# Kernel tuning notes

Hardware: AMD Instinct MI355X
Metric: run time of the kernel (lower is better)

Reference implementation:

```python
import jax, jax.numpy as jnp
import numpy as np

B, S, F, H, DK = 16, 1024, 512, 8, 64
NEG = 999999.0

def setup_inputs() -> dict:
    key = jax.random.key(0)
    ks = jax.random.split(key, 10)
    s = 1.0 / np.sqrt(F)
    inp = {
        'x': jax.random.normal(ks[0], (B, S, F), dtype=jnp.float32),
        'xlen': jax.random.randint(ks[1], (B,), 1, S + 1, dtype=jnp.int32),
        'WQw': jax.random.uniform(ks[2], (H, DK, F), jnp.float32, -s, s),
        'WQb': jax.random.uniform(ks[3], (H, DK), jnp.float32, -s, s),
        'WKw': jax.random.uniform(ks[4], (H, DK, F), jnp.float32, -s, s),
        'WKb': jax.random.uniform(ks[5], (H, DK), jnp.float32, -s, s),
        'WVw': jax.random.uniform(ks[6], (H, DK, F), jnp.float32, -s, s),
        'WVb': jax.random.uniform(ks[7], (H, DK), jnp.float32, -s, s),
        'WOw': jax.random.uniform(ks[8], (F, H * DK), jnp.float32, -1.0/np.sqrt(H*DK), 1.0/np.sqrt(H*DK)),
        'WOb': jax.random.uniform(ks[9], (F,), jnp.float32, -1.0/np.sqrt(H*DK), 1.0/np.sqrt(H*DK)),
    }
    return inp

def reference(x, xlen, WQw, WQb, WKw, WKb, WVw, WVb, WOw, WOb):
    # batched per-head projections: [B,S,F] x [H,DK,F] -> [B,H,S,DK]
    q = jnp.einsum('bsf,hdf->bhsd', x, WQw) + WQb[None, :, None, :]
    k = jnp.einsum('bsf,hdf->bhsd', x, WKw) + WKb[None, :, None, :]
    v = jnp.einsum('bsf,hdf->bhsd', x, WVw) + WVb[None, :, None, :]
    scores = jnp.einsum('bhsd,bhtd->bhst', q, k) / jnp.sqrt(jnp.float32(DK))
    # additive padding mask; original masks key positions >= xlen[j]-1 (off-by-one preserved)
    key_pos = jnp.arange(S)[None, :]                       # [1,S]
    mask = jnp.where(key_pos >= (xlen - 1)[:, None], -NEG, 0.0).astype(jnp.float32)
    scores = scores + mask[:, None, None, :]               # [B,H,S,S]
    attn = jax.nn.softmax(scores, axis=-1)
    z = jnp.einsum('bhst,bhtd->bhsd', attn, v)             # [B,H,S,DK]
    z = jnp.transpose(z, (0, 2, 1, 3)).reshape(B, S, H * DK)  # concat heads
    return z @ WOw.T + WOb
```

## Files before the change

kernel.cpp:

```cpp
#include <hip/hip_runtime.h>
#include <hip/hip_bf16.h>

typedef short bf16x8 __attribute__((ext_vector_type(8)));
typedef float f32x4 __attribute__((ext_vector_type(4)));
typedef unsigned short u16;

#define B_   16
#define S_   1024
#define F_   512
#define H_   8
#define DK_  64


__device__ __forceinline__ u16 f2bf(float f) {
    union { float f; unsigned int u; } v; v.f = f;
    return (u16)((v.u + 0x7FFFu + ((v.u >> 16) & 1u)) >> 16);
}
__device__ __forceinline__ float bf2f(u16 h) {
    union { unsigned int u; float f; } v; v.u = ((unsigned int)h) << 16;
    return v.f;
}
__device__ __forceinline__ bf16x8 cvt8(float4 a, float4 b) {
    union { u16 u[8]; bf16x8 v; } r;
    r.u[0] = f2bf(a.x); r.u[1] = f2bf(a.y); r.u[2] = f2bf(a.z); r.u[3] = f2bf(a.w);
    r.u[4] = f2bf(b.x); r.u[5] = f2bf(b.y); r.u[6] = f2bf(b.z); r.u[7] = f2bf(b.w);
    return r.v;
}
__device__ __forceinline__ unsigned int pk2(float lo, float hi) {
    union { __hip_bfloat162 h; unsigned int u; } c;
    c.h = __float22bfloat162_rn(make_float2(lo, hi));
    return c.u;
}

__device__ __forceinline__ void gl_lds16(const u16* g, u16* l) {
    __builtin_amdgcn_global_load_lds(
        (const __attribute__((address_space(1))) unsigned int*)g,
        (__attribute__((address_space(3))) unsigned int*)l,
        16, 0, 0);
}

__global__ __launch_bounds__(256) void cvt_all(
    const float* __restrict__ x,
    const float* __restrict__ wq, const float* __restrict__ wk,
    const float* __restrict__ wv, const float* __restrict__ wo,
    const float* __restrict__ bq, const float* __restrict__ bk,
    const float* __restrict__ bv, const float* __restrict__ bo,
    u16* __restrict__ Xbf, u16* __restrict__ Wbase)
{
    const size_t u = (size_t)blockIdx.x * 256 + threadIdx.x;
    const float* src; u16* dst;
    if (u < 1048576)      { src = x  + u * 8;               dst = Xbf + u * 8; }
    else if (u < 1081344) { src = wq + (u - 1048576) * 8;   dst = Wbase + (u - 1048576) * 8; }
    else if (u < 1114112) { src = wk + (u - 1081344) * 8;   dst = Wbase +  262144 + (u - 1081344) * 8; }
    else if (u < 1146880) { src = wv + (u - 1114112) * 8;   dst = Wbase +  524288 + (u - 1114112) * 8; }
    else if (u < 1179648) { src = wo + (u - 1146880) * 8;   dst = Wbase +  786432 + (u - 1146880) * 8; }
    else if (u < 1179712) { src = bq + (u - 1179648) * 8;   dst = Wbase + 1048576 + (u - 1179648) * 8; }
    else if (u < 1179776) { src = bk + (u - 1179712) * 8;   dst = Wbase + 1049088 + (u - 1179712) * 8; }
    else if (u < 1179840) { src = bv + (u - 1179776) * 8;   dst = Wbase + 1049600 + (u - 1179776) * 8; }
    else                  { src = bo + (u - 1179840) * 8;   dst = Wbase + 1050112 + (u - 1179840) * 8; }
    *(bf16x8*)dst = cvt8(*(const float4*)src, *(const float4*)(src + 4));
}

template <int EPI>
__global__ __launch_bounds__(256) void gemm128(
    const u16* __restrict__ A, const u16* __restrict__ Bm,
    const u16* __restrict__ bias, void* __restrict__ out)
{
    __shared__ __align__(16) u16 AsL[2][4096];
    __shared__ __align__(16) u16 BsL[2][4096];

    const int t    = threadIdx.x;
    const int wave = t >> 6, lane = t & 63;
    const int l15  = lane & 15, quad = lane >> 4;
    const int wr   = (wave & 1) * 64, wc = (wave >> 1) * 64;
    const int m0   = blockIdx.x * 128, n0 = blockIdx.y * 128;
    const int sr   = t >> 2, scol = (t & 3) * 8;

    float bvp[4];
#pragma unroll
    for (int j = 0; j < 4; j++) bvp[j] = bf2f(bias[n0 + wc + j * 16 + l15]);

    f32x4 acc[4][4];
#pragma unroll
    for (int i = 0; i < 4; i++)
#pragma unroll
        for (int j = 0; j < 4; j++) acc[i][j] = {0.f, 0.f, 0.f, 0.f};

    const u16* Ab = A  + (size_t)(m0 + sr) * 512 + scol;
    const u16* Bb = Bm + (size_t)(n0 + sr) * 512 + scol;

    gl_lds16(Ab,              &AsL[0][t * 8]);
    gl_lds16(Ab + 32768,      &AsL[0][2048 + t * 8]);
    gl_lds16(Bb,              &BsL[0][t * 8]);
    gl_lds16(Bb + 32768,      &BsL[0][2048 + t * 8]);
    gl_lds16(Ab + 32,         &AsL[1][t * 8]);
    gl_lds16(Ab + 32768 + 32, &AsL[1][2048 + t * 8]);
    gl_lds16(Bb + 32,         &BsL[1][t * 8]);
    gl_lds16(Bb + 32768 + 32, &BsL[1][2048 + t * 8]);

    for (int t0 = 0; t0 < 15; ++t0) {
        asm volatile("s_waitcnt vmcnt(4)" ::: "memory");
        __builtin_amdgcn_s_barrier();
        __builtin_amdgcn_sched_barrier(0);
        const int c = t0 & 1;
        bf16x8 af[4], bfv[4];
#pragma unroll
        for (int i = 0; i < 4; i++) af[i]  = *(const bf16x8*)&AsL[c][(wr + i * 16 + l15) * 32 + quad * 8];
#pragma unroll
        for (int j = 0; j < 4; j++) bfv[j] = *(const bf16x8*)&BsL[c][(wc + j * 16 + l15) * 32 + quad * 8];
#pragma unroll
        for (int i = 0; i < 4; i++)
#pragma unroll
            for (int j = 0; j < 4; j++)
                acc[i][j] = __builtin_amdgcn_mfma_f32_16x16x32_bf16(af[i], bfv[j], acc[i][j], 0, 0, 0);
        __builtin_amdgcn_sched_barrier(0);
        __builtin_amdgcn_s_barrier();
        if (t0 < 14) {
            const int k0n = (t0 + 2) * 32;
            gl_lds16(Ab + k0n,         &AsL[c][t * 8]);
            gl_lds16(Ab + 32768 + k0n, &AsL[c][2048 + t * 8]);
            gl_lds16(Bb + k0n,         &BsL[c][t * 8]);
            gl_lds16(Bb + 32768 + k0n, &BsL[c][2048 + t * 8]);
        }
    }
    asm volatile("s_waitcnt vmcnt(0)" ::: "memory");
    __builtin_amdgcn_s_barrier();
    __builtin_amdgcn_sched_barrier(0);
    {
        bf16x8 af[4], bfv[4];
#pragma unroll
        for (int i = 0; i < 4; i++) af[i]  = *(const bf16x8*)&AsL[1][(wr + i * 16 + l15) * 32 + quad * 8];
#pragma unroll
        for (int j = 0; j < 4; j++) bfv[j] = *(const bf16x8*)&BsL[1][(wc + j * 16 + l15) * 32 + quad * 8];
#pragma unroll
        for (int i = 0; i < 4; i++)
#pragma unroll
            for (int j = 0; j < 4; j++)
                acc[i][j] = __builtin_amdgcn_mfma_f32_16x16x32_bf16(af[i], bfv[j], acc[i][j], 0, 0, 0);
    }

#pragma unroll
    for (int j = 0; j < 4; j++) {
        const int n  = n0 + wc + j * 16 + l15;
        const float bv = bvp[j];
        const int hh = n >> 6, d = n & 63;
#pragma unroll
        for (int i = 0; i < 4; i++) {
#pragma unroll
            for (int r = 0; r < 4; r++) {
                const int m = m0 + wr + i * 16 + quad * 4 + r;
                const float val = acc[i][j][r] + bv;
                if (EPI == 0) {
                    const int b = m >> 10, s = m & 1023;
                    ((u16*)out)[((size_t)(b * 8 + hh) * 1024 + s) * 64 + d] = f2bf(val);
                } else if (EPI == 1) {
                    const int b = m >> 10, s = m & 1023;
                    ((u16*)out)[((size_t)(b * 8 + hh) * 64 + d) * 1024 + s] = f2bf(val);
                } else {
                    ((float*)out)[(size_t)m * 512 + n] = val;
                }
            }
        }
    }
}

__global__ __launch_bounds__(256) void attn(
    const u16* __restrict__ Xbf, const u16* __restrict__ Wqbf,
    const u16* __restrict__ bqbf,
    const u16* __restrict__ Kg, const u16* __restrict__ Vt,
    const int* __restrict__ xlen, u16* __restrict__ Z)
{
    __shared__ __align__(16) u16 smem[13824];

    const int t    = threadIdx.x;
    const int wave = t >> 6, lane = t & 63;
    const int l15  = lane & 15, quad = lane >> 4;
    const int bh   = blockIdx.y, b = bh >> 3, h = bh & 7;
    const int bx   = blockIdx.x;
    const int xm1  = xlen[b] - 1;
    const int wm   = (wave & 1) * 32, wn = (wave >> 1) * 32;

    u16* Ks = smem;
    u16* Vs = smem + 4608;
    u16* Qs = smem + 9216;

    f32x4 qa[2][2];
#pragma unroll
    for (int i = 0; i < 2; i++)
#pragma unroll
        for (int j = 0; j < 2; j++) qa[i][j] = {0.f, 0.f, 0.f, 0.f};

    const int sr = t >> 2, scol = (t & 3) * 8;
    const u16* Xb = Xbf  + (size_t)(b * 1024 + bx * 64 + sr) * 512 + scol;
    const u16* Wb = Wqbf + (size_t)(h * 64 + sr) * 512 + scol;

    float bqp[2];
#pragma unroll
    for (int j = 0; j < 2; j++) bqp[j] = bf2f(bqbf[h * 64 + wn + j * 16 + l15]);

    gl_lds16(Xb,      &smem[t * 8]);
    gl_lds16(Wb,      &smem[4096 + t * 8]);
    gl_lds16(Xb + 32, &smem[2048 + t * 8]);
    gl_lds16(Wb + 32, &smem[4096 + 2048 + t * 8]);

    for (int it = 0; it < 15; ++it) {
        asm volatile("s_waitcnt vmcnt(2)" ::: "memory");
        __builtin_amdgcn_s_barrier();
        __builtin_amdgcn_sched_barrier(0);
        const int c = it & 1;
        bf16x8 af[2], bfv[2];
#pragma unroll
        for (int i = 0; i < 2; i++) af[i]  = *(const bf16x8*)&smem[c * 2048 + (wm + i * 16 + l15) * 32 + quad * 8];
#pragma unroll
        for (int j = 0; j < 2; j++) bfv[j] = *(const bf16x8*)&smem[4096 + c * 2048 + (wn + j * 16 + l15) * 32 + quad * 8];
#pragma unroll
        for (int i = 0; i < 2; i++)
#pragma unroll
            for (int j = 0; j < 2; j++)
                qa[i][j] = __builtin_amdgcn_mfma_f32_16x16x32_bf16(af[i], bfv[j], qa[i][j], 0, 0, 0);
        __builtin_amdgcn_sched_barrier(0);
        __builtin_amdgcn_s_barrier();
        if (it < 14) {
            const int k0n = (it + 2) * 32;
            gl_lds16(Xb + k0n, &smem[c * 2048 + t * 8]);
            gl_lds16(Wb + k0n, &smem[4096 + c * 2048 + t * 8]);
        }
    }
    asm volatile("s_waitcnt vmcnt(0)" ::: "memory");
    __builtin_amdgcn_s_barrier();
    __builtin_amdgcn_sched_barrier(0);
    {
        bf16x8 af[2], bfv[2];
#pragma unroll
        for (int i = 0; i < 2; i++) af[i]  = *(const bf16x8*)&smem[2048 + (wm + i * 16 + l15) * 32 + quad * 8];
#pragma unroll
        for (int j = 0; j < 2; j++) bfv[j] = *(const bf16x8*)&smem[4096 + 2048 + (wn + j * 16 + l15) * 32 + quad * 8];
#pragma unroll
        for (int i = 0; i < 2; i++)
#pragma unroll
            for (int j = 0; j < 2; j++)
                qa[i][j] = __builtin_amdgcn_mfma_f32_16x16x32_bf16(af[i], bfv[j], qa[i][j], 0, 0, 0);
    }
#pragma unroll
    for (int j = 0; j < 2; j++) {
        const int d  = wn + j * 16 + l15;
        const float bv = bqp[j];
#pragma unroll
        for (int i = 0; i < 2; i++) {
#pragma unroll
            for (int r = 0; r < 4; r++) {
                const int row = wm + i * 16 + quad * 4 + r;
                Qs[row * 72 + d] = f2bf((qa[i][j][r] + bv) * 0.125f);
            }
        }
    }
    __syncthreads();

    bf16x8 aq[2];
#pragma unroll
    for (int kk = 0; kk < 2; kk++)
        aq[kk] = *(const bf16x8*)&Qs[(wave * 16 + l15) * 72 + kk * 32 + quad * 8];

    const size_t baseKV = (size_t)bh * (S_ * DK_);
    const bool domask = (xm1 >= 1);
    const int  Slim   = domask ? xm1 : S_;

    f32x4 o[4];
#pragma unroll
    for (int j = 0; j < 4; j++) o[j] = {0.f, 0.f, 0.f, 0.f};
    float li = 0.f;

    const int srow = t >> 3, scl = (t & 7) * 8;
    const int prow = ((srow >> 2) & 1) * 16 + (srow >> 3) * 4 + (srow & 3);

    for (int t0 = 0; t0 < Slim; t0 += 64) {
        *(uint4*)&Ks[prow * 72 + scl]        = *(const uint4*)&Kg[baseKV + (size_t)(t0 + srow) * 64 + scl];
        *(uint4*)&Ks[(prow + 32) * 72 + scl] = *(const uint4*)&Kg[baseKV + (size_t)(t0 + srow + 32) * 64 + scl];
        *(uint4*)&Vs[srow * 72 + scl]        = *(const uint4*)&Vt[baseKV + (size_t)srow * 1024 + t0 + scl];
        *(uint4*)&Vs[(srow + 32) * 72 + scl] = *(const uint4*)&Vt[baseKV + (size_t)(srow + 32) * 1024 + t0 + scl];
        __syncthreads();

        f32x4 sc[4];
#pragma unroll
        for (int nh = 0; nh < 4; nh++) {
            f32x4 s = {0.f, 0.f, 0.f, 0.f};
#pragma unroll
            for (int kk = 0; kk < 2; kk++) {
                bf16x8 bk = *(const bf16x8*)&Ks[(nh * 16 + l15) * 72 + kk * 32 + quad * 8];
                s = __builtin_amdgcn_mfma_f32_16x16x32_bf16(bk, aq[kk], s, 0, 0, 0);
            }
            sc[nh] = s;
        }
        if (domask && (t0 + 64 > xm1)) {
#pragma unroll
            for (int nh = 0; nh < 4; nh++) {
                const int kb = t0 + ((nh >> 1) << 5) + (quad << 3) + ((nh & 1) << 2);
#pragma unroll
                for (int r = 0; r < 4; r++)
                    sc[nh][r] += ((kb + r) >= xm1) ? -999999.0f : 0.0f;
            }
        }
#pragma unroll
        for (int nh = 0; nh < 4; nh++) {
#pragma unroll
            for (int r = 0; r < 4; r++) sc[nh][r] = __expf(sc[nh][r]);
            li += (sc[nh][0] + sc[nh][1]) + (sc[nh][2] + sc[nh][3]);
        }
        union { unsigned int u[4]; bf16x8 v; } ap0, ap1;
        ap0.u[0] = pk2(sc[0][0], sc[0][1]); ap0.u[1] = pk2(sc[0][2], sc[0][3]);
        ap0.u[2] = pk2(sc[1][0], sc[1][1]); ap0.u[3] = pk2(sc[1][2], sc[1][3]);
        ap1.u[0] = pk2(sc[2][0], sc[2][1]); ap1.u[1] = pk2(sc[2][2], sc[2][3]);
        ap1.u[2] = pk2(sc[3][0], sc[3][1]); ap1.u[3] = pk2(sc[3][2], sc[3][3]);
#pragma unroll
        for (int j = 0; j < 4; j++) {
            bf16x8 bv0 = *(const bf16x8*)&Vs[(j * 16 + l15) * 72 + quad * 8];
            o[j] = __builtin_amdgcn_mfma_f32_16x16x32_bf16(ap0.v, bv0, o[j], 0, 0, 0);
            bf16x8 bv1 = *(const bf16x8*)&Vs[(j * 16 + l15) * 72 + 32 + quad * 8];
            o[j] = __builtin_amdgcn_mfma_f32_16x16x32_bf16(ap1.v, bv1, o[j], 0, 0, 0);
        }
        __syncthreads();
    }

    float rs = li;
    rs += __shfl_xor(rs, 16);
    rs += __shfl_xor(rs, 32);
    const float linv = 1.0f / rs;
    float lr[4];
#pragma unroll
    for (int r = 0; r < 4; r++) lr[r] = __shfl(linv, quad * 4 + r);

#pragma unroll
    for (int j = 0; j < 4; j++) {
#pragma unroll
        for (int r = 0; r < 4; r++) {
            const int s = bx * 64 + wave * 16 + quad * 4 + r;
            Z[((size_t)(b * 1024 + s)) * 512 + h * 64 + j * 16 + l15] = f2bf(o[j][r] * lr[r]);
        }
    }
}

extern "C" void kernel_launch(void* const* d_in, const int* in_sizes, int n_in,
                              void* d_out, int out_size, void* d_ws, size_t ws_size,
                              hipStream_t stream)
{
    (void)in_sizes; (void)n_in; (void)out_size; (void)ws_size;

    const float* x    = (const float*)d_in[0];
    const int*   xlen = (const int*)d_in[1];
    const float* WQw  = (const float*)d_in[2];
    const float* WQb  = (const float*)d_in[3];
    const float* WKw  = (const float*)d_in[4];
    const float* WKb  = (const float*)d_in[5];
    const float* WVw  = (const float*)d_in[6];
    const float* WVb  = (const float*)d_in[7];
    const float* WOw  = (const float*)d_in[8];
    const float* WOb  = (const float*)d_in[9];

    const size_t NQ = (size_t)B_ * H_ * S_ * DK_;
    u16* Kb    = (u16*)d_ws;
    u16* Zb    = Kb + NQ;
    u16* Wbase = Zb + NQ;
    u16* WQbf  = Wbase;
    u16* WKbf  = Wbase + 262144;
    u16* WVbf  = Wbase + 524288;
    u16* WObf  = Wbase + 786432;
    u16* bqbf  = Wbase + 1048576;
    u16* bkbf  = Wbase + 1049088;
    u16* bvbf  = Wbase + 1049600;
    u16* bobf  = Wbase + 1050112;
    u16* Xbf = (u16*)d_out;
    u16* Vb  = Xbf + NQ;

    dim3 blk(256);
    cvt_all<<<dim3(4609), blk, 0, stream>>>(x, WQw, WKw, WVw, WOw,
                                            WQb, WKb, WVb, WOb, Xbf, Wbase);

    dim3 gGemm(128, 4);
    gemm128<0><<<gGemm, blk, 0, stream>>>(Xbf, WKbf, bkbf, Kb);
    gemm128<1><<<gGemm, blk, 0, stream>>>(Xbf, WVbf, bvbf, Vb);

    dim3 gAttn(16, 128);
    attn<<<gAttn, blk, 0, stream>>>(Xbf, WQbf, bqbf, Kb, Vb, xlen, Zb);

    gemm128<2><<<gGemm, blk, 0, stream>>>(Zb, WObf, bobf, d_out);
}
```

Baseline: 200.4 us.

## Prefetch next K/V tile into registers during attention compute

The attention loop now loads the next 64-key K and V tile from global memory into registers while the current tile is being computed, then stores it to LDS at the start of the next iteration. Raw s_barrier calls with explicit lgkmcnt waits and sched_barrier fences replace __syncthreads, so global loads can stay in flight across the barrier. The launch bounds also ask for 5 waves per SIMD, which caps register use. The aim is to hide global load latency behind the MFMA work, at the cost of more registers and possible spills under the tighter occupancy hint.

```diff
diff --git a/kernel.cpp b/kernel.cpp
--- a/kernel.cpp
+++ b/kernel.cpp
@@ -164,7 +164,7 @@
     }
 }
 
-__global__ __launch_bounds__(256) void attn(
+__global__ __launch_bounds__(256, 5) void attn(
     const u16* __restrict__ Xbf, const u16* __restrict__ Wqbf,
     const u16* __restrict__ bqbf,
     const u16* __restrict__ Kg, const u16* __restrict__ Vt,
@@ -264,6 +264,7 @@
     const size_t baseKV = (size_t)bh * (S_ * DK_);
     const bool domask = (xm1 >= 1);
     const int  Slim   = domask ? xm1 : S_;
+    const int  nt     = (Slim + 63) >> 6;
 
     f32x4 o[4];
 #pragma unroll
@@ -273,13 +274,10 @@
     const int srow = t >> 3, scl = (t & 7) * 8;
     const int prow = ((srow >> 2) & 1) * 16 + (srow >> 3) * 4 + (srow & 3);
 
-    for (int t0 = 0; t0 < Slim; t0 += 64) {
-        *(uint4*)&Ks[prow * 72 + scl]        = *(const uint4*)&Kg[baseKV + (size_t)(t0 + srow) * 64 + scl];
-        *(uint4*)&Ks[(prow + 32) * 72 + scl] = *(const uint4*)&Kg[baseKV + (size_t)(t0 + srow + 32) * 64 + scl];
-        *(uint4*)&Vs[srow * 72 + scl]        = *(const uint4*)&Vt[baseKV + (size_t)srow * 1024 + t0 + scl];
-        *(uint4*)&Vs[(srow + 32) * 72 + scl] = *(const uint4*)&Vt[baseKV + (size_t)(srow + 32) * 1024 + t0 + scl];
-        __syncthreads();
-
+    const u16* KgR = Kg + baseKV + (size_t)srow * 64 + scl;
+    const u16* VtR = Vt + baseKV + (size_t)srow * 1024 + scl;
+
+    auto tile_compute = [&](int t0) {
         f32x4 sc[4];
 #pragma unroll
         for (int nh = 0; nh < 4; nh++) {
@@ -318,7 +316,42 @@
             bf16x8 bv1 = *(const bf16x8*)&Vs[(j * 16 + l15) * 72 + 32 + quad * 8];
             o[j] = __builtin_amdgcn_mfma_f32_16x16x32_bf16(ap1.v, bv1, o[j], 0, 0, 0);
         }
-        __syncthreads();
+    };
+
+    uint4 rk0 = *(const uint4*)(KgR);
+    uint4 rk1 = *(const uint4*)(KgR + 2048);
+    uint4 rv0 = *(const uint4*)(VtR);
+    uint4 rv1 = *(const uint4*)(VtR + 32768);
+
+    for (int tt = 0; tt + 1 < nt; ++tt) {
+        const int t0 = tt << 6;
+        const int tn = t0 + 64;
+        uint4 nk0 = *(const uint4*)(KgR + (size_t)tn * 64);
+        uint4 nk1 = *(const uint4*)(KgR + (size_t)tn * 64 + 2048);
+        uint4 nv0 = *(const uint4*)(VtR + tn);
+        uint4 nv1 = *(const uint4*)(VtR + tn + 32768);
+        *(uint4*)&Ks[prow * 72 + scl]        = rk0;
+        *(uint4*)&Ks[(prow + 32) * 72 + scl] = rk1;
+        *(uint4*)&Vs[srow * 72 + scl]        = rv0;
+        *(uint4*)&Vs[(srow + 32) * 72 + scl] = rv1;
+        asm volatile("s_waitcnt lgkmcnt(0)" ::: "memory");
+        __builtin_amdgcn_s_barrier();
+        __builtin_amdgcn_sched_barrier(0);
+        tile_compute(t0);
+        __builtin_amdgcn_sched_barrier(0);
+        __builtin_amdgcn_s_barrier();
+        rk0 = nk0; rk1 = nk1; rv0 = nv0; rv1 = nv1;
+    }
+    {
+        const int t0 = (nt - 1) << 6;
+        *(uint4*)&Ks[prow * 72 + scl]        = rk0;
+        *(uint4*)&Ks[(prow + 32) * 72 + scl] = rk1;
+        *(uint4*)&Vs[srow * 72 + scl]        = rv0;
+        *(uint4*)&Vs[(srow + 32) * 72 + scl] = rv1;
+        asm volatile("s_waitcnt lgkmcnt(0)" ::: "memory");
+        __builtin_amdgcn_s_barrier();
+        __builtin_amdgcn_sched_barrier(0);
+        tile_compute(t0);
     }
 
     float rs = li;
```

Result: no change. 196.9 us (-1.8%).
